# Kernel tuning notes

Hardware: AMD Instinct MI355X
Metric: run time of the kernel (lower is better)

The kernel has to match this reference:

```python
import jax, jax.numpy as jnp
import numpy as np

N, IN, H, M, D = 2048, 400, 256, 128, 8


def setup_inputs() -> dict:
    key = jax.random.key(0)
    ks = jax.random.split(key, 20)
    g = lambda k, shp, s: jax.random.normal(k, shp, jnp.float32) * s
    C = IN // 2
    return {
        "x": g(ks[0], (N, IN), 1.0),
        "memory": g(ks[1], (N, H, M), 1.0),
        "ke_w": g(ks[2], (H, C), 1.0 / np.sqrt(C)),
        "ke_b": g(ks[3], (H,), 0.01),
        "km_w": g(ks[4], (M, H), 1.0 / np.sqrt(H)),
        "km_b": g(ks[5], (M,), 0.01),
        "kw2_w": g(ks[6], (D, H), 1.0 / np.sqrt(H)),
        "kw2_b": g(ks[7], (D,), 0.01),
        "sum_w": g(ks[8], (H, 2 * H), 1.0 / np.sqrt(2 * H)),
        "sum_b": g(ks[9], (H,), 0.01),
        "out_w": g(ks[10], (1, H), 1.0 / np.sqrt(H)),
        "out_b": g(ks[11], (1,), 0.01),
        "ve_w": g(ks[12], (H, IN), 1.0 / np.sqrt(IN)),
        "ve_b": g(ks[13], (H,), 0.01),
        "er_w": g(ks[14], (D, H, H), 1.0 / np.sqrt(H)),
        "er_b": g(ks[15], (D, H), 0.01),
        "ad_w": g(ks[16], (D, H, H), 1.0 / np.sqrt(H)),
        "ad_b": g(ks[17], (D, H), 0.01),
    }


def reference(x, memory, ke_w, ke_b, km_w, km_b, kw2_w, kw2_b,
              sum_w, sum_b, out_w, out_b, ve_w, ve_b,
              er_w, er_b, ad_w, ad_b):
    n, c2 = x.shape
    c = c2 // 2
    # query = sum of the two halves of x
    q = x.reshape(n, 2, c).sum(axis=1)                       # (N, C)
    k = q @ ke_w.T + ke_b                                    # (N, H)
    w = jax.nn.softmax(k @ km_w.T + km_b, axis=-1)           # (N, M) read/write weights
    w2 = jax.nn.softmax(k @ kw2_w.T + kw2_b, axis=-1)        # (N, D) expert gates
    # memory read: weighted sum over memory slots
    r = jnp.einsum('nhm,nm->nh', memory, w)                  # (N, H)
    f = jnp.tanh(jnp.concatenate([k, r], axis=1) @ sum_w.T + sum_b)
    y = f @ out_w.T + out_b                                  # (N, 1)
    v = x @ ve_w.T + ve_b                                    # (N, H)
    # DynamicLinear: gate-weighted mixture of per-expert linear maps
    # (fused: avoids materializing per-sample (N,H,H) weights)
    e = jax.nn.sigmoid(jnp.einsum('ni,doi,nd->no', v, er_w, w2) + w2 @ er_b)
    a = jnp.tanh(jnp.einsum('ni,doi,nd->no', v, ad_w, w2) + w2 @ ad_b)
    # memory write: erase then add
    memory = memory * (1.0 - w[:, None, :] * e[:, :, None])
    memory = memory + w[:, None, :] * a[:, :, None]
    return y, memory
```

## Files before the change

### kernel.cpp

```cpp
#include <hip/hip_runtime.h>
#include <math.h>

#define N_  2048
#define IN_ 400
#define C_  200
#define H_  256
#define M_  128
#define D_  8

#define KQ   224
#define KX   416
#define KBIG 2176
#define NZ   4
#define KSPL (KBIG / NZ)
#define KS   512

typedef __bf16 bf16x8 __attribute__((ext_vector_type(8)));
typedef float  f32x4  __attribute__((ext_vector_type(4)));

__device__ __forceinline__ ushort f2bf(float x) { __bf16 b = (__bf16)x; return __builtin_bit_cast(ushort, b); }
__device__ __forceinline__ float  bf2f(ushort u) { unsigned v = ((unsigned)u) << 16; return __builtin_bit_cast(float, v); }

#define P0 212992
#define P1 (P0 + 114688)
#define P2 (P1 + 81920)
#define P3 (P2 + 278528)
#define WC_KE (256 * KQ)
#define WC_VE (WC_KE + 256 * KX)
#define WC_SW (WC_VE + 256 * 512)
#define WC_KM (WC_SW + 128 * 256)
__global__ __launch_bounds__(256) void prep_all_kernel(
    const float* __restrict__ x,
    const float* __restrict__ ke, const float* __restrict__ ve,
    const float* __restrict__ sw, const float* __restrict__ km,
    const float* __restrict__ er_w, const float* __restrict__ er_b,
    const float* __restrict__ ad_w, const float* __restrict__ ad_b,
    ushort* __restrict__ x_bf, ushort* __restrict__ q_bf,
    ushort* __restrict__ wout, ushort* __restrict__ wcat)
{
    int idx = blockIdx.x * 256 + threadIdx.x;
    ushort pk[4];
    if (idx < P0) {
        int n = idx / (KX / 4), g = idx % (KX / 4), c0 = g * 4;
#pragma unroll
        for (int j = 0; j < 4; j++) {
            int c = c0 + j;
            pk[j] = f2bf((c < IN_) ? x[(size_t)n * IN_ + c] : 0.f);
        }
        *(ushort4*)&x_bf[(size_t)n * KX + c0] = *(ushort4*)pk;
    } else if (idx < P1) {
        int i = idx - P0;
        int n = i / (KQ / 4), g = i % (KQ / 4), c0 = g * 4;
#pragma unroll
        for (int j = 0; j < 4; j++) {
            int c = c0 + j;
            pk[j] = f2bf((c < C_) ? x[(size_t)n * IN_ + c] + x[(size_t)n * IN_ + C_ + c] : 0.f);
        }
        *(ushort4*)&q_bf[(size_t)n * KQ + c0] = *(ushort4*)pk;
    } else if (idx < P2) {
        int s0 = (idx - P1) * 4;
#pragma unroll
        for (int j = 0; j < 4; j++) {
            int s = s0 + j;
            float val;
            if (s < WC_KE)      { int r = s / KQ, c = s % KQ; val = (c < C_) ? ke[r * C_ + c] : 0.f; }
            else if (s < WC_VE) { int i = s - WC_KE; int r = i / KX, c = i % KX; val = (c < IN_) ? ve[r * IN_ + c] : 0.f; }
            else if (s < WC_SW) { val = sw[s - WC_VE]; }
            else                { val = km[s - WC_SW]; }
            pk[j] = f2bf(val);
        }
        *(ushort4*)&wout[s0] = *(ushort4*)pk;
    } else {
        int i = idx - P2;
        int o = i / (KBIG / 4), g = i % (KBIG / 4), c0 = g * 4;
        const float* Wsrc = (o < 256) ? er_w : ad_w;
        const float* bsrc = (o < 256) ? er_b : ad_b;
        int oo = o & 255;
#pragma unroll
        for (int j = 0; j < 4; j++) {
            int c = c0 + j;
            float val = 0.f;
            if (c < 2048)      { int d = c >> 8, ii = c & 255; val = Wsrc[(size_t)(d * 256 + oo) * 256 + ii]; }
            else if (c < 2056) { val = bsrc[(c - 2048) * 256 + oo]; }
            pk[j] = f2bf(val);
        }
        *(ushort4*)&wcat[(size_t)o * KBIG + c0] = *(ushort4*)pk;
    }
}

__device__ __forceinline__ void gemm_core_128x64(
    const ushort* __restrict__ A, int lda,
    const ushort* __restrict__ B, int ldb,
    const float* __restrict__ bias,
    void* __restrict__ Cv, int ldc, int outbf,
    int m0, int n0, int kFrom, int kTo,
    ushort (*As)[128][40], ushort (*Bs)[64][40])
{
    const int tid = threadIdx.x, lane = tid & 63, wave = tid >> 6;
    const int wm = (wave >> 1) * 64, wn = (wave & 1) * 32;
    const int sr = tid >> 2, sc = (tid & 3) * 8;

    f32x4 acc[4][2] = {};

    auto compute = [&](int b) {
        const int ko = (lane >> 4) * 8;
        bf16x8 af[4], bfr[2];
#pragma unroll
        for (int i = 0; i < 4; i++)
            af[i] = __builtin_bit_cast(bf16x8, *(const uint4*)&As[b][wm + i * 16 + (lane & 15)][ko]);
#pragma unroll
        for (int j = 0; j < 2; j++)
            bfr[j] = __builtin_bit_cast(bf16x8, *(const uint4*)&Bs[b][wn + j * 16 + (lane & 15)][ko]);
#pragma unroll
        for (int i = 0; i < 4; i++)
#pragma unroll
            for (int j = 0; j < 2; j++)
                acc[i][j] = __builtin_amdgcn_mfma_f32_16x16x32_bf16(af[i], bfr[j], acc[i][j], 0, 0, 0);
    };

    uint4 a0 = *(const uint4*)&A[(size_t)(m0 + sr) * lda + kFrom + sc];
    uint4 a1 = *(const uint4*)&A[(size_t)(m0 + sr + 64) * lda + kFrom + sc];
    uint4 b0 = *(const uint4*)&B[(size_t)(n0 + sr) * ldb + kFrom + sc];
    *(uint4*)&As[0][sr][sc] = a0;
    *(uint4*)&As[0][sr + 64][sc] = a1;
    *(uint4*)&Bs[0][sr][sc] = b0;
    __syncthreads();

    int cur = 0;
    for (int k0 = kFrom + 32; k0 < kTo; k0 += 32) {
        a0 = *(const uint4*)&A[(size_t)(m0 + sr) * lda + k0 + sc];
        a1 = *(const uint4*)&A[(size_t)(m0 + sr + 64) * lda + k0 + sc];
        b0 = *(const uint4*)&B[(size_t)(n0 + sr) * ldb + k0 + sc];
        compute(cur);
        *(uint4*)&As[cur ^ 1][sr][sc] = a0;
        *(uint4*)&As[cur ^ 1][sr + 64][sc] = a1;
        *(uint4*)&Bs[cur ^ 1][sr][sc] = b0;
        __syncthreads();
        cur ^= 1;
    }
    compute(cur);

    float* Cf = (float*)Cv;
    ushort* Cb = (ushort*)Cv;
#pragma unroll
    for (int i = 0; i < 4; i++) {
#pragma unroll
        for (int j = 0; j < 2; j++) {
            int row = m0 + wm + i * 16 + (lane >> 4) * 4;
            int col = n0 + wn + j * 16 + (lane & 15);
#pragma unroll
            for (int r = 0; r < 4; r++) {
                float val = acc[i][j][r];
                if (bias) val += bias[col];
                if (outbf) Cb[(size_t)(row + r) * ldc + col] = f2bf(val);
                else       Cf[(size_t)(row + r) * ldc + col] = val;
            }
        }
    }
}

__global__ __launch_bounds__(256) void kv_kernel(
    const ushort* __restrict__ q_bf, const ushort* __restrict__ ke_bf,
    const float* __restrict__ ke_b, ushort* __restrict__ kr,
    const ushort* __restrict__ x_bf, const ushort* __restrict__ ve_bf,
    const float* __restrict__ ve_b, float* __restrict__ v)
{
    __shared__ ushort As[2][128][40];
    __shared__ ushort Bs[2][64][40];
    if (blockIdx.z == 0)
        gemm_core_128x64(q_bf, KQ, ke_bf, KQ, ke_b, kr, KS, 1,
                         blockIdx.y * 128, blockIdx.x * 64, 0, KQ, As, Bs);
    else
        gemm_core_128x64(x_bf, KX, ve_bf, KX, ve_b, v, H_, 0,
                         blockIdx.y * 128, blockIdx.x * 64, 0, KX, As, Bs);
}

__global__ __launch_bounds__(256) void bigw_kernel(
    const ushort* __restrict__ vw, const ushort* __restrict__ Wcat,
    float* __restrict__ parts,
    const ushort* __restrict__ kr, const ushort* __restrict__ km_bf,
    const float* __restrict__ km_b, float* __restrict__ wlog)
{
    __shared__ ushort As[2][128][40];
    __shared__ ushort Bs[2][64][40];
    const int z = blockIdx.z;
    if (z < NZ) {
        gemm_core_128x64(vw, KBIG, Wcat, KBIG, nullptr,
                         parts + (size_t)z * N_ * 512, 512, 0,
                         blockIdx.y * 128, blockIdx.x * 64, z * KSPL, (z + 1) * KSPL, As, Bs);
    } else {
        if (blockIdx.x >= 2) return;
        gemm_core_128x64(kr, KS, km_bf, H_, km_b, wlog, M_, 0,
                         blockIdx.y * 128, blockIdx.x * 64, 0, H_, As, Bs);
    }
}

__global__ __launch_bounds__(256) void vw_kernel(
    const ushort* __restrict__ kr, const float* __restrict__ v,
    const float* __restrict__ kw2_w, const float* __restrict__ kw2_b,
    ushort* __restrict__ vw)
{
    __shared__ float kf[H_], vl[H_], lg[8], w2l[8];
    const int n = blockIdx.x, t = threadIdx.x;
    if (t < 64) {
        ushort4 u = ((const ushort4*)(kr + (size_t)n * KS))[t];
        kf[t * 4 + 0] = bf2f(u.x); kf[t * 4 + 1] = bf2f(u.y);
        kf[t * 4 + 2] = bf2f(u.z); kf[t * 4 + 3] = bf2f(u.w);
        float4 vv = ((const float4*)(v + (size_t)n * H_))[t];
        vl[t * 4 + 0] = vv.x; vl[t * 4 + 1] = vv.y;
        vl[t * 4 + 2] = vv.z; vl[t * 4 + 3] = vv.w;
    }
    __syncthreads();
    {
        int d = t >> 5, l = t & 31;
        float acc = 0.f;
        const float* wr = kw2_w + d * H_;
#pragma unroll
        for (int s = 0; s < 8; s++) acc += kf[l + 32 * s] * wr[l + 32 * s];
#pragma unroll
        for (int off = 16; off; off >>= 1) acc += __shfl_xor(acc, off);
        if (l == 0) lg[d] = acc + kw2_b[d];
    }
    __syncthreads();
    if (t < 8) {
        float val = lg[t];
        float mx = val;
#pragma unroll
        for (int off = 1; off < 8; off <<= 1) mx = fmaxf(mx, __shfl_xor(mx, off));
        float e = expf(val - mx), s = e;
#pragma unroll
        for (int off = 1; off < 8; off <<= 1) s += __shfl_xor(s, off);
        w2l[t] = e / s;
    }
    __syncthreads();
    ushort* row = vw + (size_t)n * KBIG;
    for (int g = t; g < KBIG / 4; g += 256) {
        int c0 = g * 4;
        ushort pk[4];
#pragma unroll
        for (int j = 0; j < 4; j++) {
            int c = c0 + j;
            float val = 0.f;
            if (c < 2048)      val = w2l[c >> 8] * vl[c & 255];
            else if (c < 2056) val = w2l[c - 2048];
            pk[j] = f2bf(val);
        }
        *(ushort4*)&row[c0] = *(ushort4*)pk;
    }
}

__global__ __launch_bounds__(256) void mem_stream_kernel(
    const float* __restrict__ mem_in,
    const float* __restrict__ wlog,
    const float* __restrict__ parts,
    float* __restrict__ mem_out,
    ushort* __restrict__ kr)
{
    __shared__ float wl[M_];
    __shared__ float el[128], al[128];
    __shared__ float red[4];
    const int n = blockIdx.x >> 1, half = blockIdx.x & 1, hbase = half * 128;
    const int t = threadIdx.x;

    const int col = (t < 128) ? (hbase + t) : (256 + hbase + (t - 128));
    float pacc = 0.f;
#pragma unroll
    for (int z = 0; z < NZ; z++)
        pacc += parts[(size_t)z * N_ * 512 + (size_t)n * 512 + col];

    float lv = 0.f;
    if (t < 128) {
        lv = wlog[(size_t)n * M_ + t];
        float mx = lv;
#pragma unroll
        for (int off = 32; off; off >>= 1) mx = fmaxf(mx, __shfl_xor(mx, off));
        if ((t & 63) == 0) red[t >> 6] = mx;
        el[t] = 1.f / (1.f + expf(-pacc));
    } else {
        al[t - 128] = tanhf(pacc);
    }
    __syncthreads();
    if (t < 128) {
        float gmax = fmaxf(red[0], red[1]);
        float ev = expf(lv - gmax);
        float s = ev;
#pragma unroll
        for (int off = 32; off; off >>= 1) s += __shfl_xor(s, off);
        if ((t & 63) == 0) red[2 + (t >> 6)] = s;
        wl[t] = ev;
    }
    __syncthreads();
    if (t < 128) wl[t] *= 1.f / (red[2] + red[3]);
    __syncthreads();

    const int wave = t >> 6, lane = t & 63, half2 = lane >> 5, l32 = lane & 31;
    const f32x4* min4 = (const f32x4*)(mem_in + ((size_t)n * H_ + hbase) * M_);
    f32x4* mout4 = (f32x4*)(mem_out + ((size_t)n * H_ + hbase) * M_);
    f32x4 wv = ((const f32x4*)wl)[l32];
#pragma unroll 4
    for (int i = 0; i < 16; i++) {
        int hl = i * 8 + wave * 2 + half2;
        f32x4 mv = __builtin_nontemporal_load(&min4[hl * 32 + l32]);
        float eh = el[hl], ah = al[hl];
        f32x4 nv = mv * (1.f - wv * eh) + wv * ah;
        __builtin_nontemporal_store(nv, &mout4[hl * 32 + l32]);
        float racc = mv[0] * wv[0] + mv[1] * wv[1] + mv[2] * wv[2] + mv[3] * wv[3];
#pragma unroll
        for (int off = 1; off < 32; off <<= 1) racc += __shfl_xor(racc, off);
        if (l32 == 0) kr[(size_t)n * KS + H_ + hbase + hl] = f2bf(racc);
    }
}

__global__ __launch_bounds__(256) void fy_kernel(
    const ushort* __restrict__ kr, const ushort* __restrict__ sum_bf,
    const float* __restrict__ sum_b, const float* __restrict__ out_w,
    const float* __restrict__ out_b, float* __restrict__ y)
{
    __shared__ ushort As[2][64][40];
    __shared__ ushort Bs[2][256][40];
    __shared__ float yl[64][4];
    const int tid = threadIdx.x, lane = tid & 63, wave = tid >> 6;
    const int wn = wave * 64;
    const int m0 = blockIdx.x * 64;
    const int sr = tid >> 2, sc = (tid & 3) * 8;

    f32x4 acc[4][4] = {};

    auto compute = [&](int b) {
        const int ko = (lane >> 4) * 8;
        bf16x8 af[4], bfr[4];
#pragma unroll
        for (int i = 0; i < 4; i++)
            af[i] = __builtin_bit_cast(bf16x8, *(const uint4*)&As[b][i * 16 + (lane & 15)][ko]);
#pragma unroll
        for (int j = 0; j < 4; j++)
            bfr[j] = __builtin_bit_cast(bf16x8, *(const uint4*)&Bs[b][wn + j * 16 + (lane & 15)][ko]);
#pragma unroll
        for (int i = 0; i < 4; i++)
#pragma unroll
            for (int j = 0; j < 4; j++)
                acc[i][j] = __builtin_amdgcn_mfma_f32_16x16x32_bf16(af[i], bfr[j], acc[i][j], 0, 0, 0);
    };

    uint4 a0 = *(const uint4*)&kr[(size_t)(m0 + sr) * KS + 0 + sc];
    uint4 b0 = *(const uint4*)&sum_bf[(size_t)(sr)       * KS + 0 + sc];
    uint4 b1 = *(const uint4*)&sum_bf[(size_t)(sr + 64)  * KS + 0 + sc];
    uint4 b2 = *(const uint4*)&sum_bf[(size_t)(sr + 128) * KS + 0 + sc];
    uint4 b3 = *(const uint4*)&sum_bf[(size_t)(sr + 192) * KS + 0 + sc];
    *(uint4*)&As[0][sr][sc] = a0;
    *(uint4*)&Bs[0][sr][sc] = b0;
    *(uint4*)&Bs[0][sr + 64][sc] = b1;
    *(uint4*)&Bs[0][sr + 128][sc] = b2;
    *(uint4*)&Bs[0][sr + 192][sc] = b3;
    __syncthreads();

    int cur = 0;
    for (int k0 = 32; k0 < KS; k0 += 32) {
        a0 = *(const uint4*)&kr[(size_t)(m0 + sr) * KS + k0 + sc];
        b0 = *(const uint4*)&sum_bf[(size_t)(sr)       * KS + k0 + sc];
        b1 = *(const uint4*)&sum_bf[(size_t)(sr + 64)  * KS + k0 + sc];
        b2 = *(const uint4*)&sum_bf[(size_t)(sr + 128) * KS + k0 + sc];
        b3 = *(const uint4*)&sum_bf[(size_t)(sr + 192) * KS + k0 + sc];
        compute(cur);
        *(uint4*)&As[cur ^ 1][sr][sc] = a0;
        *(uint4*)&Bs[cur ^ 1][sr][sc] = b0;
        *(uint4*)&Bs[cur ^ 1][sr + 64][sc] = b1;
        *(uint4*)&Bs[cur ^ 1][sr + 128][sc] = b2;
        *(uint4*)&Bs[cur ^ 1][sr + 192][sc] = b3;
        __syncthreads();
        cur ^= 1;
    }
    compute(cur);

    float ow[4], sb[4];
#pragma unroll
    for (int j = 0; j < 4; j++) {
        int col = wn + j * 16 + (lane & 15);
        ow[j] = out_w[col];
        sb[j] = sum_b[col];
    }
    float yp[4][4];
#pragma unroll
    for (int i = 0; i < 4; i++)
#pragma unroll
        for (int r = 0; r < 4; r++) {
            float s = 0.f;
#pragma unroll
            for (int j = 0; j < 4; j++)
                s += tanhf(acc[i][j][r] + sb[j]) * ow[j];
            yp[i][r] = s;
        }
#pragma unroll
    for (int off = 1; off < 16; off <<= 1)
#pragma unroll
        for (int i = 0; i < 4; i++)
#pragma unroll
            for (int r = 0; r < 4; r++)
                yp[i][r] += __shfl_xor(yp[i][r], off);
    if ((lane & 15) == 0) {
#pragma unroll
        for (int i = 0; i < 4; i++)
#pragma unroll
            for (int r = 0; r < 4; r++)
                yl[i * 16 + (lane >> 4) * 4 + r][wave] = yp[i][r];
    }
    __syncthreads();
    if (tid < 64)
        y[m0 + tid] = yl[tid][0] + yl[tid][1] + yl[tid][2] + yl[tid][3] + out_b[0];
}

extern "C" void kernel_launch(void* const* d_in, const int* in_sizes, int n_in,
                              void* d_out, int out_size, void* d_ws, size_t ws_size,
                              hipStream_t stream) {
    const float* x      = (const float*)d_in[0];
    const float* mem_in = (const float*)d_in[1];
    const float* ke_w   = (const float*)d_in[2];
    const float* ke_b   = (const float*)d_in[3];
    const float* km_w   = (const float*)d_in[4];
    const float* km_b   = (const float*)d_in[5];
    const float* kw2_w  = (const float*)d_in[6];
    const float* kw2_b  = (const float*)d_in[7];
    const float* sum_w  = (const float*)d_in[8];
    const float* sum_b  = (const float*)d_in[9];
    const float* out_w  = (const float*)d_in[10];
    const float* out_b  = (const float*)d_in[11];
    const float* ve_w   = (const float*)d_in[12];
    const float* ve_b   = (const float*)d_in[13];
    const float* er_w   = (const float*)d_in[14];
    const float* er_b   = (const float*)d_in[15];
    const float* ad_w   = (const float*)d_in[16];
    const float* ad_b   = (const float*)d_in[17];

    float* y_out   = (float*)d_out;
    float* mem_out = (float*)d_out + N_;

    float* ws = (float*)d_ws;
    size_t o = 0;
    float*  parts  = ws + o;            o += (size_t)NZ * N_ * 512;
    ushort* vw     = (ushort*)(ws + o); o += (size_t)N_ * KBIG / 2;
    ushort* Wcat   = (ushort*)(ws + o); o += (size_t)512 * KBIG / 2;
    ushort* kr     = (ushort*)(ws + o); o += (size_t)N_ * KS / 2;
    ushort* x_bf   = (ushort*)(ws + o); o += (size_t)N_ * KX / 2;
    ushort* q_bf   = (ushort*)(ws + o); o += (size_t)N_ * KQ / 2;
    ushort* wbf    = (ushort*)(ws + o); o += (size_t)WC_KM / 2;
    float*  v      = ws + o;            o += (size_t)N_ * H_;
    float*  wlog   = ws + o;            o += (size_t)N_ * M_;

    ushort* ke_bf  = wbf;
    ushort* ve_bf  = wbf + WC_KE;
    ushort* sum_bf = wbf + WC_VE;
    ushort* km_bf  = wbf + WC_SW;

    prep_all_kernel<<<P3 / 256, 256, 0, stream>>>(
        x, ke_w, ve_w, sum_w, km_w, er_w, er_b, ad_w, ad_b, x_bf, q_bf, wbf, Wcat);
    kv_kernel<<<dim3(4, 16, 2), 256, 0, stream>>>(
        q_bf, ke_bf, ke_b, kr, x_bf, ve_bf, ve_b, v);
    vw_kernel<<<N_, 256, 0, stream>>>(kr, v, kw2_w, kw2_b, vw);
    bigw_kernel<<<dim3(8, 16, NZ + 1), 256, 0, stream>>>(
        vw, Wcat, parts, kr, km_bf, km_b, wlog);
    mem_stream_kernel<<<2 * N_, 256, 0, stream>>>(mem_in, wlog, parts, mem_out, kr);
    fy_kernel<<<N_ / 64, 256, 0, stream>>>(kr, sum_bf, sum_b, out_w, out_b, y_out);
}
```

Measured before the change: 170.4 us.

## Fuse bf16 prep into GEMM loaders and restructure kernel launch schedule

Removes the separate prep kernel that converted x, q, and the small weight matrices to bf16. The k/v GEMMs now read fp32 x and weights directly and convert in their load lambdas, with the Wcat conversion merged into the same launch as extra z-slices. The km GEMM moves into the vw kernel, fy converts sum_w on the fly, and the big GEMM shrinks its K padding and uses more split-K slices. The aim is fewer launches and less intermediate traffic, at the cost of redundant fp32 loads and conversions inside GEMM tiles and more partial-sum buffers for mem_stream to reduce.

Measured after the change: 177.0 us. +3.9%, slower.

```diff
diff --git a/kernel.cpp b/kernel.cpp
--- a/kernel.cpp
+++ b/kernel.cpp
@@ -10,8 +10,8 @@
 
 #define KQ   224
 #define KX   416
-#define KBIG 2176
-#define NZ   4
+#define KBIG 2112
+#define NZ   6
 #define KSPL (KBIG / NZ)
 #define KS   512
 
@@ -21,61 +21,133 @@
 __device__ __forceinline__ ushort f2bf(float x) { __bf16 b = (__bf16)x; return __builtin_bit_cast(ushort, b); }
 __device__ __forceinline__ float  bf2f(ushort u) { unsigned v = ((unsigned)u) << 16; return __builtin_bit_cast(float, v); }
 
-#define P0 212992
-#define P1 (P0 + 114688)
-#define P2 (P1 + 81920)
-#define P3 (P2 + 278528)
-#define WC_KE (256 * KQ)
-#define WC_VE (WC_KE + 256 * KX)
-#define WC_SW (WC_VE + 256 * 512)
-#define WC_KM (WC_SW + 128 * 256)
-__global__ __launch_bounds__(256) void prep_all_kernel(
+__device__ __forceinline__ float4 f4z() { return make_float4(0.f, 0.f, 0.f, 0.f); }
+__device__ __forceinline__ float4 ld4p(const float* p, bool v) { return v ? *(const float4*)p : f4z(); }
+__device__ __forceinline__ float4 add4(float4 a, float4 b) {
+    return make_float4(a.x + b.x, a.y + b.y, a.z + b.z, a.w + b.w);
+}
+__device__ __forceinline__ uint4 pack8(float4 a, float4 b) {
+    ushort u[8] = { f2bf(a.x), f2bf(a.y), f2bf(a.z), f2bf(a.w),
+                    f2bf(b.x), f2bf(b.y), f2bf(b.z), f2bf(b.w) };
+    return *(uint4*)u;
+}
+
+template<class F>
+__device__ __forceinline__ void gemm_core(
+    F&& ld, const float* __restrict__ bias,
+    void* __restrict__ Cv, int ldc, int outbf,
+    int m0, int n0, int kFrom, int kTo,
+    ushort (*As)[128][40], ushort (*Bs)[64][40])
+{
+    const int tid = threadIdx.x, lane = tid & 63, wave = tid >> 6;
+    const int wm = (wave >> 1) * 64, wn = (wave & 1) * 32;
+    const int sr = tid >> 2, sc = (tid & 3) * 8;
+
+    f32x4 acc[4][2] = {};
+
+    auto compute = [&](int b) {
+        const int ko = (lane >> 4) * 8;
+        bf16x8 af[4], bfr[2];
+#pragma unroll
+        for (int i = 0; i < 4; i++)
+            af[i] = __builtin_bit_cast(bf16x8, *(const uint4*)&As[b][wm + i * 16 + (lane & 15)][ko]);
+#pragma unroll
+        for (int j = 0; j < 2; j++)
+            bfr[j] = __builtin_bit_cast(bf16x8, *(const uint4*)&Bs[b][wn + j * 16 + (lane & 15)][ko]);
+#pragma unroll
+        for (int i = 0; i < 4; i++)
+#pragma unroll
+            for (int j = 0; j < 2; j++)
+                acc[i][j] = __builtin_amdgcn_mfma_f32_16x16x32_bf16(af[i], bfr[j], acc[i][j], 0, 0, 0);
+    };
+
+    uint4 a0, a1, b0;
+    ld(kFrom, a0, a1, b0);
+    *(uint4*)&As[0][sr][sc] = a0;
+    *(uint4*)&As[0][sr + 64][sc] = a1;
+    *(uint4*)&Bs[0][sr][sc] = b0;
+    __syncthreads();
+
+    int cur = 0;
+    for (int k0 = kFrom + 32; k0 < kTo; k0 += 32) {
+        ld(k0, a0, a1, b0);
+        compute(cur);
+        *(uint4*)&As[cur ^ 1][sr][sc] = a0;
+        *(uint4*)&As[cur ^ 1][sr + 64][sc] = a1;
+        *(uint4*)&Bs[cur ^ 1][sr][sc] = b0;
+        __syncthreads();
+        cur ^= 1;
+    }
+    compute(cur);
+
+    float* Cf = (float*)Cv;
+    ushort* Cb = (ushort*)Cv;
+#pragma unroll
+    for (int i = 0; i < 4; i++) {
+#pragma unroll
+        for (int j = 0; j < 2; j++) {
+            int row = m0 + wm + i * 16 + (lane >> 4) * 4;
+            int col = n0 + wn + j * 16 + (lane & 15);
+#pragma unroll
+            for (int r = 0; r < 4; r++) {
+                float val = acc[i][j][r];
+                if (bias) val += bias[col];
+                if (outbf) Cb[(size_t)(row + r) * ldc + col] = f2bf(val);
+                else       Cf[(size_t)(row + r) * ldc + col] = val;
+            }
+        }
+    }
+}
+
+__global__ __launch_bounds__(256) void k1_kernel(
     const float* __restrict__ x,
-    const float* __restrict__ ke, const float* __restrict__ ve,
-    const float* __restrict__ sw, const float* __restrict__ km,
+    const float* __restrict__ ke_w, const float* __restrict__ ke_b, ushort* __restrict__ kr,
+    const float* __restrict__ ve_w, const float* __restrict__ ve_b, float* __restrict__ v,
     const float* __restrict__ er_w, const float* __restrict__ er_b,
     const float* __restrict__ ad_w, const float* __restrict__ ad_b,
-    ushort* __restrict__ x_bf, ushort* __restrict__ q_bf,
-    ushort* __restrict__ wout, ushort* __restrict__ wcat)
-{
-    int idx = blockIdx.x * 256 + threadIdx.x;
-    ushort pk[4];
-    if (idx < P0) {
-        int n = idx / (KX / 4), g = idx % (KX / 4), c0 = g * 4;
-#pragma unroll
-        for (int j = 0; j < 4; j++) {
-            int c = c0 + j;
-            pk[j] = f2bf((c < IN_) ? x[(size_t)n * IN_ + c] : 0.f);
-        }
-        *(ushort4*)&x_bf[(size_t)n * KX + c0] = *(ushort4*)pk;
-    } else if (idx < P1) {
-        int i = idx - P0;
-        int n = i / (KQ / 4), g = i % (KQ / 4), c0 = g * 4;
-#pragma unroll
-        for (int j = 0; j < 4; j++) {
-            int c = c0 + j;
-            pk[j] = f2bf((c < C_) ? x[(size_t)n * IN_ + c] + x[(size_t)n * IN_ + C_ + c] : 0.f);
-        }
-        *(ushort4*)&q_bf[(size_t)n * KQ + c0] = *(ushort4*)pk;
-    } else if (idx < P2) {
-        int s0 = (idx - P1) * 4;
-#pragma unroll
-        for (int j = 0; j < 4; j++) {
-            int s = s0 + j;
-            float val;
-            if (s < WC_KE)      { int r = s / KQ, c = s % KQ; val = (c < C_) ? ke[r * C_ + c] : 0.f; }
-            else if (s < WC_VE) { int i = s - WC_KE; int r = i / KX, c = i % KX; val = (c < IN_) ? ve[r * IN_ + c] : 0.f; }
-            else if (s < WC_SW) { val = sw[s - WC_VE]; }
-            else                { val = km[s - WC_SW]; }
-            pk[j] = f2bf(val);
-        }
-        *(ushort4*)&wout[s0] = *(ushort4*)pk;
+    ushort* __restrict__ wcat)
+{
+    __shared__ ushort As[2][128][40];
+    __shared__ ushort Bs[2][64][40];
+    const int z = blockIdx.z;
+    const int sr = threadIdx.x >> 2, sc = (threadIdx.x & 3) * 8;
+
+    if (z == 0) {
+        const int m0 = blockIdx.y * 128, n0 = blockIdx.x * 64;
+        auto ld = [&](int k0, uint4& A0, uint4& A1, uint4& B0) {
+            int c0 = k0 + sc, c4 = c0 + 4;
+            bool v0 = c0 < C_, v4 = c4 < C_;
+            const float* r0 = x + (size_t)(m0 + sr) * IN_;
+            const float* r1 = x + (size_t)(m0 + sr + 64) * IN_;
+            A0 = pack8(add4(ld4p(r0 + c0, v0), ld4p(r0 + C_ + c0, v0)),
+                       add4(ld4p(r0 + c4, v4), ld4p(r0 + C_ + c4, v4)));
+            A1 = pack8(add4(ld4p(r1 + c0, v0), ld4p(r1 + C_ + c0, v0)),
+                       add4(ld4p(r1 + c4, v4), ld4p(r1 + C_ + c4, v4)));
+            const float* rb = ke_w + (size_t)(n0 + sr) * C_;
+            B0 = pack8(ld4p(rb + c0, v0), ld4p(rb + c4, v4));
+        };
+        gemm_core(ld, ke_b, kr, KS, 1, m0, n0, 0, KQ, As, Bs);
+    } else if (z == 1) {
+        const int m0 = blockIdx.y * 128, n0 = blockIdx.x * 64;
+        auto ld = [&](int k0, uint4& A0, uint4& A1, uint4& B0) {
+            int c0 = k0 + sc, c4 = c0 + 4;
+            bool v0 = c0 < IN_, v4 = c4 < IN_;
+            const float* r0 = x + (size_t)(m0 + sr) * IN_;
+            const float* r1 = x + (size_t)(m0 + sr + 64) * IN_;
+            A0 = pack8(ld4p(r0 + c0, v0), ld4p(r0 + c4, v4));
+            A1 = pack8(ld4p(r1 + c0, v0), ld4p(r1 + c4, v4));
+            const float* rb = ve_w + (size_t)(n0 + sr) * IN_;
+            B0 = pack8(ld4p(rb + c0, v0), ld4p(rb + c4, v4));
+        };
+        gemm_core(ld, ve_b, v, H_, 0, m0, n0, 0, KX, As, Bs);
     } else {
-        int i = idx - P2;
-        int o = i / (KBIG / 4), g = i % (KBIG / 4), c0 = g * 4;
-        const float* Wsrc = (o < 256) ? er_w : ad_w;
-        const float* bsrc = (o < 256) ? er_b : ad_b;
-        int oo = o & 255;
+        int idx = ((z - 2) * 64 + blockIdx.y * 4 + blockIdx.x) * 256 + threadIdx.x;
+        if (idx >= 512 * (KBIG / 4)) return;
+        int oc = idx / (KBIG / 4), g = idx % (KBIG / 4), c0 = g * 4;
+        const float* Wsrc = (oc < 256) ? er_w : ad_w;
+        const float* bsrc = (oc < 256) ? er_b : ad_b;
+        int oo = oc & 255;
+        ushort pk[4];
 #pragma unroll
         for (int j = 0; j < 4; j++) {
             int c = c0 + j;
@@ -84,124 +156,36 @@
             else if (c < 2056) { val = bsrc[(c - 2048) * 256 + oo]; }
             pk[j] = f2bf(val);
         }
-        *(ushort4*)&wcat[(size_t)o * KBIG + c0] = *(ushort4*)pk;
-    }
-}
-
-__device__ __forceinline__ void gemm_core_128x64(
-    const ushort* __restrict__ A, int lda,
-    const ushort* __restrict__ B, int ldb,
-    const float* __restrict__ bias,
-    void* __restrict__ Cv, int ldc, int outbf,
-    int m0, int n0, int kFrom, int kTo,
-    ushort (*As)[128][40], ushort (*Bs)[64][40])
-{
-    const int tid = threadIdx.x, lane = tid & 63, wave = tid >> 6;
-    const int wm = (wave >> 1) * 64, wn = (wave & 1) * 32;
-    const int sr = tid >> 2, sc = (tid & 3) * 8;
-
-    f32x4 acc[4][2] = {};
-
-    auto compute = [&](int b) {
-        const int ko = (lane >> 4) * 8;
-        bf16x8 af[4], bfr[2];
-#pragma unroll
-        for (int i = 0; i < 4; i++)
-            af[i] = __builtin_bit_cast(bf16x8, *(const uint4*)&As[b][wm + i * 16 + (lane & 15)][ko]);
-#pragma unroll
-        for (int j = 0; j < 2; j++)
-            bfr[j] = __builtin_bit_cast(bf16x8, *(const uint4*)&Bs[b][wn + j * 16 + (lane & 15)][ko]);
-#pragma unroll
-        for (int i = 0; i < 4; i++)
-#pragma unroll
-            for (int j = 0; j < 2; j++)
-                acc[i][j] = __builtin_amdgcn_mfma_f32_16x16x32_bf16(af[i], bfr[j], acc[i][j], 0, 0, 0);
-    };
-
-    uint4 a0 = *(const uint4*)&A[(size_t)(m0 + sr) * lda + kFrom + sc];
-    uint4 a1 = *(const uint4*)&A[(size_t)(m0 + sr + 64) * lda + kFrom + sc];
-    uint4 b0 = *(const uint4*)&B[(size_t)(n0 + sr) * ldb + kFrom + sc];
-    *(uint4*)&As[0][sr][sc] = a0;
-    *(uint4*)&As[0][sr + 64][sc] = a1;
-    *(uint4*)&Bs[0][sr][sc] = b0;
-    __syncthreads();
-
-    int cur = 0;
-    for (int k0 = kFrom + 32; k0 < kTo; k0 += 32) {
-        a0 = *(const uint4*)&A[(size_t)(m0 + sr) * lda + k0 + sc];
-        a1 = *(const uint4*)&A[(size_t)(m0 + sr + 64) * lda + k0 + sc];
-        b0 = *(const uint4*)&B[(size_t)(n0 + sr) * ldb + k0 + sc];
-        compute(cur);
-        *(uint4*)&As[cur ^ 1][sr][sc] = a0;
-        *(uint4*)&As[cur ^ 1][sr + 64][sc] = a1;
-        *(uint4*)&Bs[cur ^ 1][sr][sc] = b0;
-        __syncthreads();
-        cur ^= 1;
-    }
-    compute(cur);
-
-    float* Cf = (float*)Cv;
-    ushort* Cb = (ushort*)Cv;
-#pragma unroll
-    for (int i = 0; i < 4; i++) {
-#pragma unroll
-        for (int j = 0; j < 2; j++) {
-            int row = m0 + wm + i * 16 + (lane >> 4) * 4;
-            int col = n0 + wn + j * 16 + (lane & 15);
-#pragma unroll
-            for (int r = 0; r < 4; r++) {
-                float val = acc[i][j][r];
-                if (bias) val += bias[col];
-                if (outbf) Cb[(size_t)(row + r) * ldc + col] = f2bf(val);
-                else       Cf[(size_t)(row + r) * ldc + col] = val;
-            }
-        }
-    }
-}
-
-__global__ __launch_bounds__(256) void kv_kernel(
-    const ushort* __restrict__ q_bf, const ushort* __restrict__ ke_bf,
-    const float* __restrict__ ke_b, ushort* __restrict__ kr,
-    const ushort* __restrict__ x_bf, const ushort* __restrict__ ve_bf,
-    const float* __restrict__ ve_b, float* __restrict__ v)
+        *(ushort4*)&wcat[(size_t)oc * KBIG + c0] = *(ushort4*)pk;
+    }
+}
+
+__global__ __launch_bounds__(256) void vww_kernel(
+    const ushort* __restrict__ kr, const float* __restrict__ v,
+    const float* __restrict__ kw2_w, const float* __restrict__ kw2_b,
+    const float* __restrict__ km_w, const float* __restrict__ km_b,
+    float* __restrict__ wlog, ushort* __restrict__ vw)
 {
     __shared__ ushort As[2][128][40];
     __shared__ ushort Bs[2][64][40];
-    if (blockIdx.z == 0)
-        gemm_core_128x64(q_bf, KQ, ke_bf, KQ, ke_b, kr, KS, 1,
-                         blockIdx.y * 128, blockIdx.x * 64, 0, KQ, As, Bs);
-    else
-        gemm_core_128x64(x_bf, KX, ve_bf, KX, ve_b, v, H_, 0,
-                         blockIdx.y * 128, blockIdx.x * 64, 0, KX, As, Bs);
-}
-
-__global__ __launch_bounds__(256) void bigw_kernel(
-    const ushort* __restrict__ vw, const ushort* __restrict__ Wcat,
-    float* __restrict__ parts,
-    const ushort* __restrict__ kr, const ushort* __restrict__ km_bf,
-    const float* __restrict__ km_b, float* __restrict__ wlog)
-{
-    __shared__ ushort As[2][128][40];
-    __shared__ ushort Bs[2][64][40];
-    const int z = blockIdx.z;
-    if (z < NZ) {
-        gemm_core_128x64(vw, KBIG, Wcat, KBIG, nullptr,
-                         parts + (size_t)z * N_ * 512, 512, 0,
-                         blockIdx.y * 128, blockIdx.x * 64, z * KSPL, (z + 1) * KSPL, As, Bs);
-    } else {
-        if (blockIdx.x >= 2) return;
-        gemm_core_128x64(kr, KS, km_bf, H_, km_b, wlog, M_, 0,
-                         blockIdx.y * 128, blockIdx.x * 64, 0, H_, As, Bs);
-    }
-}
-
-__global__ __launch_bounds__(256) void vw_kernel(
-    const ushort* __restrict__ kr, const float* __restrict__ v,
-    const float* __restrict__ kw2_w, const float* __restrict__ kw2_b,
-    ushort* __restrict__ vw)
-{
     __shared__ float kf[H_], vl[H_], lg[8], w2l[8];
-    const int n = blockIdx.x, t = threadIdx.x;
+    const int b = blockIdx.x, t = threadIdx.x;
+    const int sr = t >> 2, sc = (t & 3) * 8;
+
+    if (b < 32) {
+        const int m0 = (b >> 1) * 128, n0 = (b & 1) * 64;
+        auto ld = [&](int k0, uint4& A0, uint4& A1, uint4& B0) {
+            A0 = *(const uint4*)&kr[(size_t)(m0 + sr) * KS + k0 + sc];
+            A1 = *(const uint4*)&kr[(size_t)(m0 + sr + 64) * KS + k0 + sc];
+            int c0 = k0 + sc, c4 = c0 + 4;
+            const float* rb = km_w + (size_t)(n0 + sr) * H_;
+            B0 = pack8(*(const float4*)(rb + c0), *(const float4*)(rb + c4));
+        };
+        gemm_core(ld, km_b, wlog, M_, 0, m0, n0, 0, H_, As, Bs);
+        return;
+    }
+
+    const int n = b - 32;
     if (t < 64) {
         ushort4 u = ((const ushort4*)(kr + (size_t)n * KS))[t];
         kf[t * 4 + 0] = bf2f(u.x); kf[t * 4 + 1] = bf2f(u.y);
@@ -249,6 +233,24 @@
     }
 }
 
+__global__ __launch_bounds__(256) void bigw_kernel(
+    const ushort* __restrict__ vw, const ushort* __restrict__ Wcat,
+    float* __restrict__ parts)
+{
+    __shared__ ushort As[2][128][40];
+    __shared__ ushort Bs[2][64][40];
+    const int z = blockIdx.z;
+    const int m0 = blockIdx.y * 128, n0 = blockIdx.x * 64;
+    const int sr = threadIdx.x >> 2, sc = (threadIdx.x & 3) * 8;
+    auto ld = [&](int k0, uint4& A0, uint4& A1, uint4& B0) {
+        A0 = *(const uint4*)&vw[(size_t)(m0 + sr) * KBIG + k0 + sc];
+        A1 = *(const uint4*)&vw[(size_t)(m0 + sr + 64) * KBIG + k0 + sc];
+        B0 = *(const uint4*)&Wcat[(size_t)(n0 + sr) * KBIG + k0 + sc];
+    };
+    gemm_core(ld, nullptr, parts + (size_t)z * N_ * 512, 512, 0,
+              m0, n0, z * KSPL, (z + 1) * KSPL, As, Bs);
+}
+
 __global__ __launch_bounds__(256) void mem_stream_kernel(
     const float* __restrict__ mem_in,
     const float* __restrict__ wlog,
@@ -300,7 +302,7 @@
 #pragma unroll 4
     for (int i = 0; i < 16; i++) {
         int hl = i * 8 + wave * 2 + half2;
-        f32x4 mv = __builtin_nontemporal_load(&min4[hl * 32 + l32]);
+        f32x4 mv = min4[hl * 32 + l32];
         float eh = el[hl], ah = al[hl];
         f32x4 nv = mv * (1.f - wv * eh) + wv * ah;
         __builtin_nontemporal_store(nv, &mout4[hl * 32 + l32]);
@@ -312,7 +314,7 @@
 }
 
 __global__ __launch_bounds__(256) void fy_kernel(
-    const ushort* __restrict__ kr, const ushort* __restrict__ sum_bf,
+    const ushort* __restrict__ kr, const float* __restrict__ sum_w,
     const float* __restrict__ sum_b, const float* __restrict__ out_w,
     const float* __restrict__ out_b, float* __restrict__ y)
 {
@@ -342,31 +344,22 @@
                 acc[i][j] = __builtin_amdgcn_mfma_f32_16x16x32_bf16(af[i], bfr[j], acc[i][j], 0, 0, 0);
     };
 
-    uint4 a0 = *(const uint4*)&kr[(size_t)(m0 + sr) * KS + 0 + sc];
-    uint4 b0 = *(const uint4*)&sum_bf[(size_t)(sr)       * KS + 0 + sc];
-    uint4 b1 = *(const uint4*)&sum_bf[(size_t)(sr + 64)  * KS + 0 + sc];
-    uint4 b2 = *(const uint4*)&sum_bf[(size_t)(sr + 128) * KS + 0 + sc];
-    uint4 b3 = *(const uint4*)&sum_bf[(size_t)(sr + 192) * KS + 0 + sc];
-    *(uint4*)&As[0][sr][sc] = a0;
-    *(uint4*)&Bs[0][sr][sc] = b0;
-    *(uint4*)&Bs[0][sr + 64][sc] = b1;
-    *(uint4*)&Bs[0][sr + 128][sc] = b2;
-    *(uint4*)&Bs[0][sr + 192][sc] = b3;
-    __syncthreads();
-
+    auto stage = [&](int buf, int k0) {
+        int c0 = k0 + sc, c4 = c0 + 4;
+        *(uint4*)&As[buf][sr][sc] = *(const uint4*)&kr[(size_t)(m0 + sr) * KS + k0 + sc];
+#pragma unroll
+        for (int g = 0; g < 4; g++) {
+            const float* rb = sum_w + (size_t)(sr + g * 64) * KS;
+            *(uint4*)&Bs[buf][sr + g * 64][sc] = pack8(*(const float4*)(rb + c0), *(const float4*)(rb + c4));
+        }
+    };
+
+    stage(0, 0);
+    __syncthreads();
     int cur = 0;
     for (int k0 = 32; k0 < KS; k0 += 32) {
-        a0 = *(const uint4*)&kr[(size_t)(m0 + sr) * KS + k0 + sc];
-        b0 = *(const uint4*)&sum_bf[(size_t)(sr)       * KS + k0 + sc];
-        b1 = *(const uint4*)&sum_bf[(size_t)(sr + 64)  * KS + k0 + sc];
-        b2 = *(const uint4*)&sum_bf[(size_t)(sr + 128) * KS + k0 + sc];
-        b3 = *(const uint4*)&sum_bf[(size_t)(sr + 192) * KS + k0 + sc];
         compute(cur);
-        *(uint4*)&As[cur ^ 1][sr][sc] = a0;
-        *(uint4*)&Bs[cur ^ 1][sr][sc] = b0;
-        *(uint4*)&Bs[cur ^ 1][sr + 64][sc] = b1;
-        *(uint4*)&Bs[cur ^ 1][sr + 128][sc] = b2;
-        *(uint4*)&Bs[cur ^ 1][sr + 192][sc] = b3;
+        stage(cur ^ 1, k0);
         __syncthreads();
         cur ^= 1;
     }
@@ -436,28 +429,18 @@
 
     float* ws = (float*)d_ws;
     size_t o = 0;
-    float*  parts  = ws + o;            o += (size_t)NZ * N_ * 512;
-    ushort* vw     = (ushort*)(ws + o); o += (size_t)N_ * KBIG / 2;
-    ushort* Wcat   = (ushort*)(ws + o); o += (size_t)512 * KBIG / 2;
-    ushort* kr     = (ushort*)(ws + o); o += (size_t)N_ * KS / 2;
-    ushort* x_bf   = (ushort*)(ws + o); o += (size_t)N_ * KX / 2;
-    ushort* q_bf   = (ushort*)(ws + o); o += (size_t)N_ * KQ / 2;
-    ushort* wbf    = (ushort*)(ws + o); o += (size_t)WC_KM / 2;
-    float*  v      = ws + o;            o += (size_t)N_ * H_;
-    float*  wlog   = ws + o;            o += (size_t)N_ * M_;
-
-    ushort* ke_bf  = wbf;
-    ushort* ve_bf  = wbf + WC_KE;
-    ushort* sum_bf = wbf + WC_VE;
-    ushort* km_bf  = wbf + WC_SW;
-
-    prep_all_kernel<<<P3 / 256, 256, 0, stream>>>(
-        x, ke_w, ve_w, sum_w, km_w, er_w, er_b, ad_w, ad_b, x_bf, q_bf, wbf, Wcat);
-    kv_kernel<<<dim3(4, 16, 2), 256, 0, stream>>>(
-        q_bf, ke_bf, ke_b, kr, x_bf, ve_bf, ve_b, v);
-    vw_kernel<<<N_, 256, 0, stream>>>(kr, v, kw2_w, kw2_b, vw);
-    bigw_kernel<<<dim3(8, 16, NZ + 1), 256, 0, stream>>>(
-        vw, Wcat, parts, kr, km_bf, km_b, wlog);
+    float*  parts = ws + o;            o += (size_t)NZ * N_ * 512;
+    ushort* vw    = (ushort*)(ws + o); o += (size_t)N_ * KBIG / 2;
+    ushort* Wcat  = (ushort*)(ws + o); o += (size_t)512 * KBIG / 2;
+    ushort* kr    = (ushort*)(ws + o); o += (size_t)N_ * KS / 2;
+    float*  v     = ws + o;            o += (size_t)N_ * H_;
+    float*  wlog  = ws + o;            o += (size_t)N_ * M_;
+
+    k1_kernel<<<dim3(4, 16, 19), 256, 0, stream>>>(
+        x, ke_w, ke_b, kr, ve_w, ve_b, v, er_w, er_b, ad_w, ad_b, Wcat);
+    vww_kernel<<<32 + N_, 256, 0, stream>>>(
+        kr, v, kw2_w, kw2_b, km_w, km_b, wlog, vw);
+    bigw_kernel<<<dim3(8, 16, NZ), 256, 0, stream>>>(vw, Wcat, parts);
     mem_stream_kernel<<<2 * N_, 256, 0, stream>>>(mem_in, wlog, parts, mem_out, kr);
-    fy_kernel<<<N_ / 64, 256, 0, stream>>>(kr, sum_bf, sum_b, out_w, out_b, y_out);
-}
+    fy_kernel<<<N_ / 64, 256, 0, stream>>>(kr, sum_w, sum_b, out_w, out_b, y_out);
+}
```
